# Kernel optimization log

Hardware: AMD Instinct MI355X
Metric: run time of the kernel (lower is better)

## Reference

```python
import jax, jax.numpy as jnp
import numpy as np

ROWS = 256
COLS = 256
EPS = 1e-8


def _radius_bins(rows, cols):
    # Same construction as SpectralLoss.__init__: integer radius per rfft bin,
    # ifftshifted along the row axis to match torch.rfft layout.
    shift_rows = rows // 2
    cols_onesided = cols // 2 + 1
    idx = np.indices((rows, cols_onesided)) - np.array([[[shift_rows]], [[0]]])
    r = np.sqrt(idx[0] ** 2 + idx[1] ** 2).astype(int)
    r = np.fft.ifftshift(r, axes=0)
    return r  # [rows, cols_onesided], values in [0, r_max]


def setup_inputs() -> dict:
    key = jax.random.key(0)
    k1, k2 = jax.random.split(key)
    r = _radius_bins(ROWS, COLS)
    vector_length = int(r.max()) + 1  # 182
    data = jax.random.normal(k1, (128, 3, ROWS, COLS), dtype=jnp.float32)
    mean = jax.random.uniform(k2, (vector_length,), dtype=jnp.float32)
    radius = jnp.asarray(r, dtype=jnp.int32)
    return {"data": data, "mean": mean, "radius": radius}


def reference(data, mean, radius):
    L = mean.shape[0]  # vector_length = r_max + 1
    # RGB -> luma (as in SpectralLoss.fft)
    gray = 0.299 * data[:, 0] + 0.587 * data[:, 1] + 0.114 * data[:, 2]  # [B,H,W]
    f = jnp.fft.rfft2(gray)  # [B, H, W//2+1]
    power = f.real ** 2 + f.imag ** 2  # sum of squared re/im parts
    fft_abs = 20.0 * jnp.log(power + EPS)  # [B, H, Wc]
    # Radial histogram: segment-mean keyed on integer radius (replaces the
    # original dense one-hot mask broadcast of shape [B, L, H, Wc]).
    seg = radius.reshape(-1)  # [N] with N = H*Wc
    B = fft_abs.shape[0]
    flat = fft_abs.reshape(B, -1).T  # [N, B]
    sums = jax.ops.segment_sum(flat, seg, num_segments=L)  # [L, B]
    counts = jax.ops.segment_sum(jnp.ones_like(flat[:, :1]), seg, num_segments=L)  # [L, 1]
    profile = (sums / counts).T  # [B, L]
    # Per-sample min-max normalization (same order of ops as torch code)
    profile = profile - jnp.min(profile, axis=1, keepdims=True)
    profile = profile / jnp.max(profile, axis=1, keepdims=True)
    # L1 loss with reduction='sum' against the target mean profile
    return jnp.sum(jnp.abs(profile - mean[None, :]))
```

## Files before the change

kernel.cpp:

```cpp
#include <hip/hip_runtime.h>
#include <cmath>

#define B_   128
#define H_   256
#define W_   256
#define WC_  129
#define L_   182
#define NG_  33
#define PI_F 3.14159265358979f

__device__ __forceinline__ void fft256_wave(float vr[4], float vi[4], int l) {
  float c0, s0;
  __sincosf(-2.f * PI_F * (float)l / 256.f, &s0, &c0);
  {
    float ur = vr[0] + vr[2], ui = vi[0] + vi[2];
    float dr = vr[0] - vr[2], di = vi[0] - vi[2];
    vr[0] = ur; vi[0] = ui;
    vr[2] = dr * c0 - di * s0; vi[2] = dr * s0 + di * c0;
    float c1 = s0, s1 = -c0;
    ur = vr[1] + vr[3]; ui = vi[1] + vi[3];
    dr = vr[1] - vr[3]; di = vi[1] - vi[3];
    vr[1] = ur; vi[1] = ui;
    vr[3] = dr * c1 - di * s1; vi[3] = dr * s1 + di * c1;
  }
  {
    float c2 = c0 * c0 - s0 * s0, s2 = 2.f * c0 * s0;
    float ur = vr[0] + vr[1], ui = vi[0] + vi[1];
    float dr = vr[0] - vr[1], di = vi[0] - vi[1];
    vr[0] = ur; vi[0] = ui;
    vr[1] = dr * c2 - di * s2; vi[1] = dr * s2 + di * c2;
    ur = vr[2] + vr[3]; ui = vi[2] + vi[3];
    dr = vr[2] - vr[3]; di = vi[2] - vi[3];
    vr[2] = ur; vi[2] = ui;
    vr[3] = dr * c2 - di * s2; vi[3] = dr * s2 + di * c2;
  }
  #pragma unroll
  for (int h = 32; h >= 1; h >>= 1) {
    int i = l & (h - 1);
    float c, s;
    __sincosf(-PI_F * (float)i / (float)h, &s, &c);
    bool up = (l & h) != 0;
    float cc = up ? c : 1.f;
    float ss = up ? s : 0.f;
    float sgn = up ? -1.f : 1.f;
    #pragma unroll
    for (int j = 0; j < 4; ++j) {
      float br = __shfl_xor(vr[j], h, 64);
      float bi = __shfl_xor(vi[j], h, 64);
      float tr = fmaf(sgn, vr[j], br);
      float ti = fmaf(sgn, vi[j], bi);
      vr[j] = tr * cc - ti * ss;
      vi[j] = tr * ss + ti * cc;
    }
  }
}

#define P1_PAIRS 16
#define P1_STRIDE 259

__global__ __launch_bounds__(1024) void pass1_kernel(
    const float* __restrict__ data, float4* __restrict__ inter4) {
  __shared__ float2 tile[P1_PAIRS * P1_STRIDE];
  int tid = threadIdx.x;
  int w = tid >> 6, l = tid & 63;
  int b = blockIdx.x >> 3;
  int row0 = (blockIdx.x & 7) * 32;
  int rowA = row0 + 2 * w;
  const float* pA = data + ((size_t)b * 3) * (H_ * W_) + (size_t)rowA * W_;
  float vr[4], vi[4];
  #pragma unroll
  for (int j = 0; j < 4; ++j) {
    int i = l + 64 * j;
    float r = pA[i], g = pA[H_ * W_ + i], bl = pA[2 * H_ * W_ + i];
    vr[j] = fmaf(0.299f, r, fmaf(0.587f, g, 0.114f * bl));
    r = pA[W_ + i]; g = pA[H_ * W_ + W_ + i]; bl = pA[2 * H_ * W_ + W_ + i];
    vi[j] = fmaf(0.299f, r, fmaf(0.587f, g, 0.114f * bl));
  }
  fft256_wave(vr, vi, l);
  #pragma unroll
  for (int j = 0; j < 4; ++j)
    tile[w * P1_STRIDE + l + 64 * j] = make_float2(vr[j], vi[j]);
  __syncthreads();
  for (int f = tid; f < WC_ * P1_PAIRS; f += 1024) {
    int k = f >> 4;
    int p = f & 15;
    int qk  = (int)(__brev((unsigned)k) >> 24);
    int qnk = (int)(__brev((unsigned)((256 - k) & 255)) >> 24);
    float2 Zk  = tile[p * P1_STRIDE + qk];
    float2 Znk = tile[p * P1_STRIDE + qnk];
    float4 o;
    o.x = 0.5f * (Zk.x + Znk.x);
    o.y = 0.5f * (Zk.y - Znk.y);
    o.z = 0.5f * (Zk.y + Znk.y);
    o.w = 0.5f * (Znk.x - Zk.x);
    inter4[((((size_t)b * WC_ + k) * H_ + row0) >> 1) + p] = o;
  }
}

__global__ __launch_bounds__(256) void pass2_kernel(
    const float2* __restrict__ inter, const int* __restrict__ radius,
    float* __restrict__ partial, float* __restrict__ cntpart) {
  __shared__ float lbins[L_];
  __shared__ float lcnt[L_];
  int tid = threadIdx.x;
  int wv = tid >> 6, l = tid & 63;
  int b = blockIdx.x / NG_;
  int g = blockIdx.x - b * NG_;
  int k = g * 4 + wv;
  bool do_cnt = (b == 0);
  for (int i = tid; i < L_; i += 256) lbins[i] = 0.f;
  if (do_cnt)
    for (int i = tid; i < L_; i += 256) lcnt[i] = 0.f;
  __syncthreads();
  if (k < WC_) {
    const float2* p = inter + ((size_t)b * WC_ + k) * H_;
    float vr[4], vi[4];
    #pragma unroll
    for (int j = 0; j < 4; ++j) {
      float2 v = p[l + 64 * j];
      vr[j] = v.x; vi[j] = v.y;
    }
    fft256_wave(vr, vi, l);
    int rb = 4 * (int)(__brev((unsigned)l) >> 26);
    #pragma unroll
    for (int j = 0; j < 4; ++j) {
      int rf = rb + ((j == 1) ? 2 : (j == 2) ? 1 : j);
      int bin = radius[rf * WC_ + k];
      float pw = vr[j] * vr[j] + vi[j] * vi[j];
      float val = 20.f * __logf(pw + 1e-8f);
      atomicAdd(&lbins[bin], val);
      if (do_cnt) atomicAdd(&lcnt[bin], 1.f);
    }
  }
  __syncthreads();
  float* pp = partial + ((size_t)b * NG_ + g) * L_;
  for (int i = tid; i < L_; i += 256) pp[i] = lbins[i];
  if (do_cnt) {
    float* cp = cntpart + (size_t)g * L_;
    for (int i = tid; i < L_; i += 256) cp[i] = lcnt[i];
  }
}

__global__ __launch_bounds__(256) void loss_kernel(
    const float* __restrict__ partial, const float* __restrict__ cntpart,
    const float* __restrict__ mean, float* __restrict__ lpart) {
  int b = blockIdx.x;
  int t = threadIdx.x;
  __shared__ float prof[L_];
  __shared__ float red[256];
  float acc = 0.f, csum = 0.f;
  if (t < L_) {
    const float* pb = partial + (size_t)b * NG_ * L_;
    #pragma unroll 3
    for (int g = 0; g < NG_; ++g) {
      acc  += pb[g * L_ + t];
      csum += cntpart[g * L_ + t];
    }
    prof[t] = acc / csum;
  }
  __syncthreads();
  red[t] = (t < L_) ? prof[t] : INFINITY;
  __syncthreads();
  for (int s = 128; s > 0; s >>= 1) {
    if (t < s) red[t] = fminf(red[t], red[t + s]);
    __syncthreads();
  }
  float mn = red[0];
  __syncthreads();
  red[t] = (t < L_) ? (prof[t] - mn) : -INFINITY;
  __syncthreads();
  for (int s = 128; s > 0; s >>= 1) {
    if (t < s) red[t] = fmaxf(red[t], red[t + s]);
    __syncthreads();
  }
  float mx = red[0];
  __syncthreads();
  red[t] = (t < L_) ? fabsf((prof[t] - mn) / mx - mean[t]) : 0.f;
  __syncthreads();
  for (int s = 128; s > 0; s >>= 1) {
    if (t < s) red[t] += red[t + s];
    __syncthreads();
  }
  if (t == 0) lpart[b] = red[0];
}

__global__ __launch_bounds__(64) void final_kernel(
    const float* __restrict__ lpart, float* __restrict__ out) {
  int l = threadIdx.x;
  float v = lpart[l] + lpart[l + 64];
  #pragma unroll
  for (int h = 32; h >= 1; h >>= 1) v += __shfl_xor(v, h, 64);
  if (l == 0) out[0] = v;
}

extern "C" void kernel_launch(void* const* d_in, const int* in_sizes, int n_in,
                              void* d_out, int out_size, void* d_ws, size_t ws_size,
                              hipStream_t stream) {
  const float* data   = (const float*)d_in[0];
  const float* mean   = (const float*)d_in[1];
  const int*   radius = (const int*)d_in[2];
  float* out = (float*)d_out;

  float2* inter = (float2*)d_ws;
  size_t inter_bytes = (size_t)B_ * WC_ * H_ * sizeof(float2);
  float* partial = (float*)((char*)d_ws + inter_bytes);
  float* cntpart = partial + (size_t)B_ * NG_ * L_;
  float* lpart   = cntpart + (size_t)NG_ * L_;

  pass1_kernel<<<B_ * 8, 1024, 0, stream>>>(data, (float4*)inter);
  pass2_kernel<<<B_ * NG_, 256, 0, stream>>>(inter, radius, partial, cntpart);
  loss_kernel<<<B_, 256, 0, stream>>>(partial, cntpart, mean, lpart);
  final_kernel<<<1, 64, 0, stream>>>(lpart, out);
}
```

Baseline: 194.3 us.

## Fuse column FFT pass with loss reduction, one block per batch

Replaces the 33-way split per batch plus separate loss kernel with one 1024-thread block per batch. Each block runs all 129 column FFTs, bins them in shared memory, and does the min/max/L1 reduction in a single wave. Bin counts are now computed once by block 0 of pass1 instead of in pass2. This removes the partial-sum buffer, its write and re-read, and one kernel launch. The cost is that pass2 now launches only 128 blocks, which may leave many CUs idle and lower memory throughput while reading the intermediate spectrum.

After: 251.4 us. 1.29x slower.

```diff
diff --git a/kernel.cpp b/kernel.cpp
--- a/kernel.cpp
+++ b/kernel.cpp
@@ -6,7 +6,6 @@
 #define W_   256
 #define WC_  129
 #define L_   182
-#define NG_  33
 #define PI_F 3.14159265358979f
 
 __device__ __forceinline__ void fft256_wave(float vr[4], float vi[4], int l) {
@@ -59,9 +58,13 @@
 #define P1_STRIDE 259
 
 __global__ __launch_bounds__(1024) void pass1_kernel(
-    const float* __restrict__ data, float4* __restrict__ inter4) {
+    const float* __restrict__ data, float4* __restrict__ inter4,
+    const int* __restrict__ radius, float* __restrict__ cnt) {
   __shared__ float2 tile[P1_PAIRS * P1_STRIDE];
+  __shared__ float lcnt[L_];
   int tid = threadIdx.x;
+  bool blk0 = (blockIdx.x == 0);
+  if (blk0 && tid < L_) lcnt[tid] = 0.f;
   int w = tid >> 6, l = tid & 63;
   int b = blockIdx.x >> 3;
   int row0 = (blockIdx.x & 7) * 32;
@@ -95,24 +98,27 @@
     o.w = 0.5f * (Znk.x - Zk.x);
     inter4[((((size_t)b * WC_ + k) * H_ + row0) >> 1) + p] = o;
   }
+  if (blk0) {
+    int base = tid * 33;
+    int end  = base + 33;
+    if (end > H_ * WC_) end = H_ * WC_;
+    for (int i = base; i < end; ++i) atomicAdd(&lcnt[radius[i]], 1.f);
+    __syncthreads();
+    if (tid < L_) cnt[tid] = lcnt[tid];
+  }
 }
 
-__global__ __launch_bounds__(256) void pass2_kernel(
+__global__ __launch_bounds__(1024) void pass2_loss_kernel(
     const float2* __restrict__ inter, const int* __restrict__ radius,
-    float* __restrict__ partial, float* __restrict__ cntpart) {
+    const float* __restrict__ cnt, const float* __restrict__ mean,
+    float* __restrict__ lpart) {
   __shared__ float lbins[L_];
-  __shared__ float lcnt[L_];
   int tid = threadIdx.x;
   int wv = tid >> 6, l = tid & 63;
-  int b = blockIdx.x / NG_;
-  int g = blockIdx.x - b * NG_;
-  int k = g * 4 + wv;
-  bool do_cnt = (b == 0);
-  for (int i = tid; i < L_; i += 256) lbins[i] = 0.f;
-  if (do_cnt)
-    for (int i = tid; i < L_; i += 256) lcnt[i] = 0.f;
+  int b = blockIdx.x;
+  if (tid < L_) lbins[tid] = 0.f;
   __syncthreads();
-  if (k < WC_) {
+  for (int k = wv; k < WC_; k += 16) {
     const float2* p = inter + ((size_t)b * WC_ + k) * H_;
     float vr[4], vi[4];
     #pragma unroll
@@ -125,63 +131,34 @@
     #pragma unroll
     for (int j = 0; j < 4; ++j) {
       int rf = rb + ((j == 1) ? 2 : (j == 2) ? 1 : j);
-      int bin = radius[rf * WC_ + k];
       float pw = vr[j] * vr[j] + vi[j] * vi[j];
       float val = 20.f * __logf(pw + 1e-8f);
-      atomicAdd(&lbins[bin], val);
-      if (do_cnt) atomicAdd(&lcnt[bin], 1.f);
+      atomicAdd(&lbins[radius[rf * WC_ + k]], val);
     }
   }
   __syncthreads();
-  float* pp = partial + ((size_t)b * NG_ + g) * L_;
-  for (int i = tid; i < L_; i += 256) pp[i] = lbins[i];
-  if (do_cnt) {
-    float* cp = cntpart + (size_t)g * L_;
-    for (int i = tid; i < L_; i += 256) cp[i] = lcnt[i];
+  if (wv == 0) {
+    float pr[3];
+    #pragma unroll
+    for (int u = 0; u < 3; ++u) {
+      int idx = l + 64 * u;
+      pr[u] = (idx < L_) ? lbins[idx] / cnt[idx] : 0.f;
+    }
+    float mn = fminf(pr[0], pr[1]);
+    if (l < L_ - 128) mn = fminf(mn, pr[2]);
+    #pragma unroll
+    for (int h = 32; h >= 1; h >>= 1) mn = fminf(mn, __shfl_xor(mn, h, 64));
+    float mx = fmaxf(pr[0] - mn, pr[1] - mn);
+    if (l < L_ - 128) mx = fmaxf(mx, pr[2] - mn);
+    #pragma unroll
+    for (int h = 32; h >= 1; h >>= 1) mx = fmaxf(mx, __shfl_xor(mx, h, 64));
+    float s = fabsf((pr[0] - mn) / mx - mean[l]) +
+              fabsf((pr[1] - mn) / mx - mean[l + 64]);
+    if (l < L_ - 128) s += fabsf((pr[2] - mn) / mx - mean[l + 128]);
+    #pragma unroll
+    for (int h = 32; h >= 1; h >>= 1) s += __shfl_xor(s, h, 64);
+    if (l == 0) lpart[b] = s;
   }
-}
-
-__global__ __launch_bounds__(256) void loss_kernel(
-    const float* __restrict__ partial, const float* __restrict__ cntpart,
-    const float* __restrict__ mean, float* __restrict__ lpart) {
-  int b = blockIdx.x;
-  int t = threadIdx.x;
-  __shared__ float prof[L_];
-  __shared__ float red[256];
-  float acc = 0.f, csum = 0.f;
-  if (t < L_) {
-    const float* pb = partial + (size_t)b * NG_ * L_;
-    #pragma unroll 3
-    for (int g = 0; g < NG_; ++g) {
-      acc  += pb[g * L_ + t];
-      csum += cntpart[g * L_ + t];
-    }
-    prof[t] = acc / csum;
-  }
-  __syncthreads();
-  red[t] = (t < L_) ? prof[t] : INFINITY;
-  __syncthreads();
-  for (int s = 128; s > 0; s >>= 1) {
-    if (t < s) red[t] = fminf(red[t], red[t + s]);
-    __syncthreads();
-  }
-  float mn = red[0];
-  __syncthreads();
-  red[t] = (t < L_) ? (prof[t] - mn) : -INFINITY;
-  __syncthreads();
-  for (int s = 128; s > 0; s >>= 1) {
-    if (t < s) red[t] = fmaxf(red[t], red[t + s]);
-    __syncthreads();
-  }
-  float mx = red[0];
-  __syncthreads();
-  red[t] = (t < L_) ? fabsf((prof[t] - mn) / mx - mean[t]) : 0.f;
-  __syncthreads();
-  for (int s = 128; s > 0; s >>= 1) {
-    if (t < s) red[t] += red[t + s];
-    __syncthreads();
-  }
-  if (t == 0) lpart[b] = red[0];
 }
 
 __global__ __launch_bounds__(64) void final_kernel(
@@ -203,12 +180,10 @@
 
   float2* inter = (float2*)d_ws;
   size_t inter_bytes = (size_t)B_ * WC_ * H_ * sizeof(float2);
-  float* partial = (float*)((char*)d_ws + inter_bytes);
-  float* cntpart = partial + (size_t)B_ * NG_ * L_;
-  float* lpart   = cntpart + (size_t)NG_ * L_;
+  float* cnt   = (float*)((char*)d_ws + inter_bytes);
+  float* lpart = cnt + L_;
 
-  pass1_kernel<<<B_ * 8, 1024, 0, stream>>>(data, (float4*)inter);
-  pass2_kernel<<<B_ * NG_, 256, 0, stream>>>(inter, radius, partial, cntpart);
-  loss_kernel<<<B_, 256, 0, stream>>>(partial, cntpart, mean, lpart);
+  pass1_kernel<<<B_ * 8, 1024, 0, stream>>>(data, (float4*)inter, radius, cnt);
+  pass2_loss_kernel<<<B_, 1024, 0, stream>>>(inter, radius, cnt, mean, lpart);
   final_kernel<<<1, 64, 0, stream>>>(lpart, out);
 }
```

## Restructure row FFT pass: four row-pairs per wave with float4 loads

Applied to the files above, without the earlier changes.

The first-pass kernel now has each wave transform four packed row pairs instead of one. Blocks shrink from 1024 to 256 threads. Each lane loads contiguous float4 chunks, which changes the FFT data layout to a different decomposition: six shuffle stages whose twiddles are built by recurrence from one sincos, followed by an in-register radix-4 stage. The shared-memory readout index is remapped to match the new element order. This cuts the number of sincos calls and issues wider, coalesced global loads, but raises register pressure and lowers occupancy per block.

Measured after the change: 196.8 us. No clear change (+1.3%).

```diff
diff --git a/kernel.cpp b/kernel.cpp
--- a/kernel.cpp
+++ b/kernel.cpp
@@ -55,39 +55,111 @@
   }
 }
 
-#define P1_PAIRS 16
+__device__ __forceinline__ void stage4(float (&vr)[4][4], float (&vi)[4][4],
+                                       int l, int h, float CT, float ST) {
+  int i = l & (h - 1);
+  float s, c;
+  __sincosf(-PI_F * (float)i / (float)h, &s, &c);
+  float wr[4], wi[4];
+  wr[0] = c;                    wi[0] = s;
+  wr[1] = c * CT + s * ST;      wi[1] = s * CT - c * ST;
+  wr[2] = wr[1] * CT + wi[1] * ST; wi[2] = wi[1] * CT - wr[1] * ST;
+  wr[3] = wr[2] * CT + wi[2] * ST; wi[3] = wi[2] * CT - wr[2] * ST;
+  bool up = (l & h) != 0;
+  float sgn = up ? -1.f : 1.f;
+  #pragma unroll
+  for (int f = 0; f < 4; ++f) {
+    #pragma unroll
+    for (int j = 0; j < 4; ++j) {
+      float br = __shfl_xor(vr[f][j], h, 64);
+      float bi = __shfl_xor(vi[f][j], h, 64);
+      float tr = fmaf(sgn, vr[f][j], br);
+      float ti = fmaf(sgn, vi[f][j], bi);
+      float cc = up ? wr[j] : 1.f;
+      float ss = up ? wi[j] : 0.f;
+      vr[f][j] = tr * cc - ti * ss;
+      vi[f][j] = tr * ss + ti * cc;
+    }
+  }
+}
+
+__device__ __forceinline__ float4 luma4(float4 r, float4 g, float4 b) {
+  float4 o;
+  o.x = fmaf(0.299f, r.x, fmaf(0.587f, g.x, 0.114f * b.x));
+  o.y = fmaf(0.299f, r.y, fmaf(0.587f, g.y, 0.114f * b.y));
+  o.z = fmaf(0.299f, r.z, fmaf(0.587f, g.z, 0.114f * b.z));
+  o.w = fmaf(0.299f, r.w, fmaf(0.587f, g.w, 0.114f * b.w));
+  return o;
+}
+
 #define P1_STRIDE 259
 
-__global__ __launch_bounds__(1024) void pass1_kernel(
+__global__ __launch_bounds__(256) void pass1_kernel(
     const float* __restrict__ data, float4* __restrict__ inter4) {
-  __shared__ float2 tile[P1_PAIRS * P1_STRIDE];
+  __shared__ float2 tile[16 * P1_STRIDE];
   int tid = threadIdx.x;
   int w = tid >> 6, l = tid & 63;
   int b = blockIdx.x >> 3;
-  int row0 = (blockIdx.x & 7) * 32;
-  int rowA = row0 + 2 * w;
-  const float* pA = data + ((size_t)b * 3) * (H_ * W_) + (size_t)rowA * W_;
-  float vr[4], vi[4];
-  #pragma unroll
-  for (int j = 0; j < 4; ++j) {
-    int i = l + 64 * j;
-    float r = pA[i], g = pA[H_ * W_ + i], bl = pA[2 * H_ * W_ + i];
-    vr[j] = fmaf(0.299f, r, fmaf(0.587f, g, 0.114f * bl));
-    r = pA[W_ + i]; g = pA[H_ * W_ + W_ + i]; bl = pA[2 * H_ * W_ + W_ + i];
-    vi[j] = fmaf(0.299f, r, fmaf(0.587f, g, 0.114f * bl));
-  }
-  fft256_wave(vr, vi, l);
-  #pragma unroll
-  for (int j = 0; j < 4; ++j)
-    tile[w * P1_STRIDE + l + 64 * j] = make_float2(vr[j], vi[j]);
-  __syncthreads();
-  for (int f = tid; f < WC_ * P1_PAIRS; f += 1024) {
-    int k = f >> 4;
-    int p = f & 15;
-    int qk  = (int)(__brev((unsigned)k) >> 24);
-    int qnk = (int)(__brev((unsigned)((256 - k) & 255)) >> 24);
-    float2 Zk  = tile[p * P1_STRIDE + qk];
-    float2 Znk = tile[p * P1_STRIDE + qnk];
+  int rg = blockIdx.x & 7;
+  int row0 = rg * 32;
+  const float* img = data + ((size_t)b * 3) * (H_ * W_);
+  float vr[4][4], vi[4][4];
+  #pragma unroll
+  for (int half = 0; half < 2; ++half) {
+    float4 ra[2], ga[2], ba[2], rb[2], gb[2], bb[2];
+    #pragma unroll
+    for (int e = 0; e < 2; ++e) {
+      int f = half * 2 + e;
+      int rowA = row0 + 2 * (4 * w + f);
+      const float* pA = img + (size_t)rowA * W_ + 4 * l;
+      ra[e] = *(const float4*)(pA);
+      ga[e] = *(const float4*)(pA + H_ * W_);
+      ba[e] = *(const float4*)(pA + 2 * H_ * W_);
+      rb[e] = *(const float4*)(pA + W_);
+      gb[e] = *(const float4*)(pA + H_ * W_ + W_);
+      bb[e] = *(const float4*)(pA + 2 * H_ * W_ + W_);
+    }
+    #pragma unroll
+    for (int e = 0; e < 2; ++e) {
+      int f = half * 2 + e;
+      float4 A = luma4(ra[e], ga[e], ba[e]);
+      float4 Bv = luma4(rb[e], gb[e], bb[e]);
+      vr[f][0] = A.x; vr[f][1] = A.y; vr[f][2] = A.z; vr[f][3] = A.w;
+      vi[f][0] = Bv.x; vi[f][1] = Bv.y; vi[f][2] = Bv.z; vi[f][3] = Bv.w;
+    }
+  }
+  stage4(vr, vi, l, 32, 0.9996988187f, 0.0245412285f);
+  stage4(vr, vi, l, 16, 0.9987954562f, 0.0490676743f);
+  stage4(vr, vi, l,  8, 0.9951847267f, 0.0980171403f);
+  stage4(vr, vi, l,  4, 0.9807852804f, 0.1950903220f);
+  stage4(vr, vi, l,  2, 0.9238795325f, 0.3826834324f);
+  stage4(vr, vi, l,  1, 0.7071067812f, 0.7071067812f);
+  #pragma unroll
+  for (int f = 0; f < 4; ++f) {
+    float u0r = vr[f][0] + vr[f][2], u0i = vi[f][0] + vi[f][2];
+    float v0r = vr[f][0] - vr[f][2], v0i = vi[f][0] - vi[f][2];
+    float u1r = vr[f][1] + vr[f][3], u1i = vi[f][1] + vi[f][3];
+    float d1r = vr[f][1] - vr[f][3], d1i = vi[f][1] - vi[f][3];
+    float v1r = d1i, v1i = -d1r;
+    vr[f][0] = u0r + u1r; vi[f][0] = u0i + u1i;
+    vr[f][1] = u0r - u1r; vi[f][1] = u0i - u1i;
+    vr[f][2] = v0r + v1r; vi[f][2] = v0i + v1i;
+    vr[f][3] = v0r - v1r; vi[f][3] = v0i - v1i;
+    int p = 4 * w + f;
+    #pragma unroll
+    for (int j = 0; j < 4; ++j)
+      tile[p * P1_STRIDE + l + 64 * j] = make_float2(vr[f][j], vi[f][j]);
+  }
+  __syncthreads();
+  for (int fi = tid; fi < WC_ * 16; fi += 256) {
+    int k = fi >> 4;
+    int p = fi & 15;
+    int q  = (int)(__brev((unsigned)k) >> 24);
+    int qn = (int)(__brev((unsigned)((256 - k) & 255)) >> 24);
+    int qs  = (q >> 2)  + 64 * (q & 3);
+    int qns = (qn >> 2) + 64 * (qn & 3);
+    float2 Zk  = tile[p * P1_STRIDE + qs];
+    float2 Znk = tile[p * P1_STRIDE + qns];
     float4 o;
     o.x = 0.5f * (Zk.x + Znk.x);
     o.y = 0.5f * (Zk.y - Znk.y);
@@ -207,7 +279,7 @@
   float* cntpart = partial + (size_t)B_ * NG_ * L_;
   float* lpart   = cntpart + (size_t)NG_ * L_;
 
-  pass1_kernel<<<B_ * 8, 1024, 0, stream>>>(data, (float4*)inter);
+  pass1_kernel<<<B_ * 8, 256, 0, stream>>>(data, (float4*)inter);
   pass2_kernel<<<B_ * NG_, 256, 0, stream>>>(inter, radius, partial, cntpart);
   loss_kernel<<<B_, 256, 0, stream>>>(partial, cntpart, mean, lpart);
   final_kernel<<<1, 64, 0, stream>>>(lpart, out);
```
